# Performance work log

Measured on AMD Instinct MI355X. Metric: run time of the kernel, lower is better.

The kernel has to match this reference:

```python
import jax, jax.numpy as jnp
import numpy as np

N_NODES = 100000
N_EDGES = 3200000
IN_CH = 128
HID_CH = 64
NEG_SLOPE = 0.2  # PyG GATConv default leaky_relu slope


def setup_inputs() -> dict:
    key = jax.random.key(0)
    k1, k2, k3, k4, k5, k6 = jax.random.split(key, 6)
    x = jax.random.normal(k1, (N_NODES, IN_CH), dtype=jnp.float32)
    edge_index = jax.random.randint(k2, (2, N_EDGES), 0, N_NODES, dtype=jnp.int64)
    # learned params of GATConv(in, hid, heads=1)
    W = jax.random.normal(k3, (IN_CH, HID_CH), dtype=jnp.float32) / np.sqrt(IN_CH)
    att_src = jax.random.normal(k4, (HID_CH,), dtype=jnp.float32) / np.sqrt(HID_CH)
    att_dst = jax.random.normal(k5, (HID_CH,), dtype=jnp.float32) / np.sqrt(HID_CH)
    bias = jax.random.normal(k6, (HID_CH,), dtype=jnp.float32) * 0.01
    return {"x": x, "edge_index": edge_index, "W": W, "att_src": att_src,
            "att_dst": att_dst, "bias": bias}


def reference(x, edge_index, W, att_src, att_dst, bias):
    N = x.shape[0]
    h = x @ W  # [N, H] linear transform
    # PyG GATConv default: add self loops
    loops = jnp.arange(N, dtype=edge_index.dtype)
    src = jnp.concatenate([edge_index[0], loops])  # [E+N]
    dst = jnp.concatenate([edge_index[1], loops])
    # per-node attention halves, then gather per-edge
    a_src = h @ att_src  # [N]
    a_dst = h @ att_dst  # [N]
    e = jax.nn.leaky_relu(a_src[src] + a_dst[dst], NEG_SLOPE)  # [E+N]
    # segment softmax over incoming edges of each destination node
    m = jax.ops.segment_max(e, dst, num_segments=N)
    e = jnp.exp(e - m[dst])
    s = jax.ops.segment_sum(e, dst, num_segments=N)
    alpha = e / s[dst]  # [E+N]
    # scatter-aggregate weighted source features
    out = jax.ops.segment_sum(h[src] * alpha[:, None], dst, num_segments=N) + bias
    return out, alpha[:, None]
```

## Files before the change

### kernel.cpp

```cpp
#include <hip/hip_runtime.h>
#include <hip/hip_bf16.h>

#define IN_CH 128
#define HID 64
#define NEG_SLOPE 0.2f
#define BSH 9
#define CAP 18432

typedef __attribute__((ext_vector_type(8))) short short8;
typedef __attribute__((ext_vector_type(4))) float floatx4;

__device__ inline short bfr(float f) {
    unsigned u = __float_as_uint(f);
    u += 0x7fffu + ((u >> 16) & 1u);
    return (short)(u >> 16);
}

__global__ void k_prep(const float* __restrict__ W, short* __restrict__ wfrag)
{
    int idx = blockIdx.x * 256 + threadIdx.x;
    if (idx >= 1024) return;
    int f = idx >> 6, l = idx & 63;
    int kt = f >> 2, nt = f & 3;
    int k0 = kt * 32 + (l >> 4) * 8;
    int n = nt * 16 + (l & 15);
#pragma unroll
    for (int j = 0; j < 8; ++j)
        wfrag[idx * 8 + j] = bfr(W[(k0 + j) * HID + n]);
}

__global__ __launch_bounds__(256) void k_gemm(
    const float* __restrict__ x, const short8* __restrict__ wfrag,
    const float* __restrict__ att_src, const float* __restrict__ att_dst,
    short* __restrict__ h, float* __restrict__ a_src,
    float* __restrict__ a_dst, int N)
{
    const int t = threadIdx.x;
    const int lane = t & 63;
    const int wv = t >> 6;
    const int l15 = lane & 15;
    const int quad = lane >> 4;

    short8 bf[16];
#pragma unroll
    for (int f = 0; f < 16; ++f) bf[f] = wfrag[f * 64 + lane];

    float as4[4], ad4[4];
#pragma unroll
    for (int nt = 0; nt < 4; ++nt) {
        as4[nt] = att_src[nt * 16 + l15];
        ad4[nt] = att_dst[nt * 16 + l15];
    }

    const int rowbase = blockIdx.x * 128 + wv * 32;

#pragma unroll
    for (int mt = 0; mt < 2; ++mt) {
        const int m0 = rowbase + mt * 16;
        const int rowa = m0 + l15;
        const int rowc = rowa < N ? rowa : N - 1;
        const float* xp = x + (size_t)rowc * IN_CH + quad * 8;

        short8 af[4];
#pragma unroll
        for (int kt = 0; kt < 4; ++kt) {
            float4 p0 = *(const float4*)(xp + kt * 32);
            float4 p1 = *(const float4*)(xp + kt * 32 + 4);
            short8 a;
            a[0] = bfr(p0.x); a[1] = bfr(p0.y); a[2] = bfr(p0.z); a[3] = bfr(p0.w);
            a[4] = bfr(p1.x); a[5] = bfr(p1.y); a[6] = bfr(p1.z); a[7] = bfr(p1.w);
            af[kt] = a;
        }

        floatx4 acc[4];
#pragma unroll
        for (int nt = 0; nt < 4; ++nt) acc[nt] = (floatx4){0.f, 0.f, 0.f, 0.f};
#pragma unroll
        for (int kt = 0; kt < 4; ++kt)
#pragma unroll
            for (int nt = 0; nt < 4; ++nt)
                acc[nt] = __builtin_amdgcn_mfma_f32_16x16x32_bf16(
                    af[kt], bf[kt * 4 + nt], acc[nt], 0, 0, 0);

#pragma unroll
        for (int r = 0; r < 4; ++r) {
            const int row = m0 + quad * 4 + r;
            const bool ok = row < N;
            if (ok) {
#pragma unroll
                for (int nt = 0; nt < 4; ++nt)
                    h[(size_t)row * HID + nt * 16 + l15] = bfr(acc[nt][r]);
            }
            float ps = acc[0][r] * as4[0] + acc[1][r] * as4[1] +
                       acc[2][r] * as4[2] + acc[3][r] * as4[3];
            float pd = acc[0][r] * ad4[0] + acc[1][r] * ad4[1] +
                       acc[2][r] * ad4[2] + acc[3][r] * ad4[3];
#pragma unroll
            for (int m2 = 1; m2 < 16; m2 <<= 1) {
                ps += __shfl_xor(ps, m2, 64);
                pd += __shfl_xor(pd, m2, 64);
            }
            if (ok && l15 == 0) { a_src[row] = ps; a_dst[row] = pd; }
        }
    }
}

__global__ __launch_bounds__(256) void k_binB(
    const int* __restrict__ ei, int* __restrict__ g_cursor,
    int* __restrict__ pairs, int E, int nb)
{
    __shared__ int hist[256];
    __shared__ int base[256];
    const int t = threadIdx.x;
    hist[t] = 0;
    __syncthreads();

    int s[16], d[16];
    const int4* s4 = (const int4*)ei;
    const int4* d4 = (const int4*)(ei + E);
    const int E4 = E >> 2;
    const int q0 = blockIdx.x * 1024;
#pragma unroll
    for (int i = 0; i < 4; ++i) {
        int q = q0 + i * 256 + t;
        int4 sv = make_int4(0, 0, 0, 0);
        int4 dv = make_int4(-1, -1, -1, -1);
        if (q < E4) { sv = s4[q]; dv = d4[q]; }
        s[4 * i + 0] = sv.x; s[4 * i + 1] = sv.y; s[4 * i + 2] = sv.z; s[4 * i + 3] = sv.w;
        d[4 * i + 0] = dv.x; d[4 * i + 1] = dv.y; d[4 * i + 2] = dv.z; d[4 * i + 3] = dv.w;
    }
#pragma unroll
    for (int i = 0; i < 16; ++i)
        if (d[i] >= 0) atomicAdd(&hist[d[i] >> BSH], 1);
    __syncthreads();

    if (t < nb) base[t] = atomicAdd(&g_cursor[t], hist[t]);
    __syncthreads();
    hist[t] = 0;
    __syncthreads();

#pragma unroll
    for (int i = 0; i < 16; ++i) {
        if (d[i] < 0) continue;
        int b = d[i] >> BSH;
        int l = atomicAdd(&hist[b], 1);
        int pos = base[b] + l;
        if (pos < CAP)
            pairs[b * CAP + pos] = s[i] | ((d[i] & 511) << 17);
    }
}

__global__ __launch_bounds__(256) void k_bscan(
    const int* __restrict__ g_cursor, int* __restrict__ bucket_base, int nb)
{
    __shared__ int sh[256];
    const int t = threadIdx.x;
    int v = (t < nb) ? g_cursor[t] : 0;
    sh[t] = v;
    __syncthreads();
    for (int off = 1; off < 256; off <<= 1) {
        int u = (t >= off) ? sh[t - off] : 0;
        __syncthreads();
        sh[t] += u;
        __syncthreads();
    }
    if (t < nb) bucket_base[t] = sh[t] - v;
}

__global__ __launch_bounds__(512) void k_binC(
    const int* __restrict__ pairs, const int* __restrict__ g_cursor,
    const int* __restrict__ bucket_base,
    int* __restrict__ row_start, int* __restrict__ cnt,
    int* __restrict__ csr_src, int N)
{
    __shared__ int h0[512];
    __shared__ int hs[512];
    __shared__ int cur[512];
    const int t = threadIdx.x;
    const int b = blockIdx.x;
    const int d0 = b << BSH;
    const int m = g_cursor[b];
    const int basec = bucket_base[b];
    const int* pb = pairs + b * CAP;

    h0[t] = 0;
    __syncthreads();
    for (int i = t; i < m; i += 512)
        atomicAdd(&h0[pb[i] >> 17], 1);
    __syncthreads();

    hs[t] = h0[t];
    __syncthreads();
    for (int off = 1; off < 512; off <<= 1) {
        int u = (t >= off) ? hs[t - off] : 0;
        __syncthreads();
        hs[t] += u;
        __syncthreads();
    }
    const int excl = hs[t] - h0[t];
    cur[t] = basec + excl;
    const int dd = d0 + t;
    if (dd < N) { row_start[dd] = basec + excl; cnt[dd] = h0[t]; }
    __syncthreads();

    for (int i = t; i < m; i += 512) {
        int p = pb[i];
        int pos = atomicAdd(&cur[p >> 17], 1);
        csr_src[pos] = p & 0x1FFFF;
    }
}

__global__ __launch_bounds__(256) void k_agg(
    const __hip_bfloat16* __restrict__ h, const float* __restrict__ a_src,
    const float* __restrict__ a_dst, const float* __restrict__ bias,
    const int* __restrict__ row_start, const int* __restrict__ cnt,
    const int* __restrict__ csr_src,
    float* __restrict__ out, float* __restrict__ inv_s, int N)
{
    const int wave = threadIdx.x >> 6;
    const int lane = threadIdx.x & 63;
    const int d = blockIdx.x * 4 + wave;
    if (d >= N) return;

    const int q  = lane >> 3;
    const int i8 = lane & 7;

    const float ad = a_dst[d];
    const int start = row_start[d];
    const int n = cnt[d];
    const int end = start + n;

    const uint4* h4 = (const uint4*)h;

    float psum = 0.f;
    float acc[8];
#pragma unroll
    for (int c = 0; c < 8; ++c) acc[c] = 0.f;

    for (int b = start; b < end; b += 64) {
        int idx = b + lane;
        int s = 0;
        float e = 0.f;
        if (idx < end) {
            s = csr_src[idx];
            float v = a_src[s] + ad;
            v = v > 0.f ? v : NEG_SLOPE * v;
            e = __expf(v);
            psum += e;
        }
        const int m = min(64, end - b);
#pragma unroll 4
        for (int j = 0; j < m; j += 8) {
            const int jq = j + q;
            const int sj = __shfl(s, jq, 64);
            const float ej = __shfl(e, jq, 64);
            uint4 u = h4[(size_t)sj * 8 + i8];
            acc[0] = fmaf(ej, __uint_as_float(u.x << 16),          acc[0]);
            acc[1] = fmaf(ej, __uint_as_float(u.x & 0xffff0000u),  acc[1]);
            acc[2] = fmaf(ej, __uint_as_float(u.y << 16),          acc[2]);
            acc[3] = fmaf(ej, __uint_as_float(u.y & 0xffff0000u),  acc[3]);
            acc[4] = fmaf(ej, __uint_as_float(u.z << 16),          acc[4]);
            acc[5] = fmaf(ej, __uint_as_float(u.z & 0xffff0000u),  acc[5]);
            acc[6] = fmaf(ej, __uint_as_float(u.w << 16),          acc[6]);
            acc[7] = fmaf(ej, __uint_as_float(u.w & 0xffff0000u),  acc[7]);
        }
    }

#pragma unroll
    for (int m2 = 32; m2 > 0; m2 >>= 1) psum += __shfl_xor(psum, m2, 64);

    float vs = a_src[d] + ad;
    vs = vs > 0.f ? vs : NEG_SLOPE * vs;
    const float eself = __expf(vs);
    const float inv = 1.0f / (psum + eself);
    if (lane == 0) inv_s[d] = inv;

#pragma unroll
    for (int c = 0; c < 8; ++c) {
        acc[c] += __shfl_xor(acc[c], 8, 64);
        acc[c] += __shfl_xor(acc[c], 16, 64);
        acc[c] += __shfl_xor(acc[c], 32, 64);
    }

    if (q == 0) {
        uint4 u = h4[(size_t)d * 8 + i8];
        float hc[8];
        hc[0] = __uint_as_float(u.x << 16);
        hc[1] = __uint_as_float(u.x & 0xffff0000u);
        hc[2] = __uint_as_float(u.y << 16);
        hc[3] = __uint_as_float(u.y & 0xffff0000u);
        hc[4] = __uint_as_float(u.z << 16);
        hc[5] = __uint_as_float(u.z & 0xffff0000u);
        hc[6] = __uint_as_float(u.w << 16);
        hc[7] = __uint_as_float(u.w & 0xffff0000u);
        float4 b0 = ((const float4*)bias)[2 * i8];
        float4 b1 = ((const float4*)bias)[2 * i8 + 1];
        float4 o0, o1;
        o0.x = fmaf(eself, hc[0], acc[0]) * inv + b0.x;
        o0.y = fmaf(eself, hc[1], acc[1]) * inv + b0.y;
        o0.z = fmaf(eself, hc[2], acc[2]) * inv + b0.z;
        o0.w = fmaf(eself, hc[3], acc[3]) * inv + b0.w;
        o1.x = fmaf(eself, hc[4], acc[4]) * inv + b1.x;
        o1.y = fmaf(eself, hc[5], acc[5]) * inv + b1.y;
        o1.z = fmaf(eself, hc[6], acc[6]) * inv + b1.z;
        o1.w = fmaf(eself, hc[7], acc[7]) * inv + b1.w;
        float* op = out + (size_t)d * HID + 8 * i8;
        *(float4*)op       = o0;
        *(float4*)(op + 4) = o1;
    }
}

__global__ void k_alpha(const int* __restrict__ ei,
                        const float* __restrict__ a_src,
                        const float* __restrict__ a_dst,
                        const float* __restrict__ inv_s,
                        float* __restrict__ out_alpha, int E, int N)
{
    int e = blockIdx.x * 256 + threadIdx.x;
    if (e >= E + N) return;
    int s, d;
    if (e < E) { s = ei[e]; d = ei[E + e]; }
    else       { s = e - E; d = s; }
    float v = a_src[s] + a_dst[d];
    v = v > 0.f ? v : NEG_SLOPE * v;
    out_alpha[e] = __expf(v) * inv_s[d];
}

extern "C" void kernel_launch(void* const* d_in, const int* in_sizes, int n_in,
                              void* d_out, int out_size, void* d_ws, size_t ws_size,
                              hipStream_t stream)
{
    (void)n_in; (void)out_size; (void)ws_size;
    const float* x       = (const float*)d_in[0];
    const int*   ei      = (const int*)d_in[1];
    const float* W       = (const float*)d_in[2];
    const float* att_src = (const float*)d_in[3];
    const float* att_dst = (const float*)d_in[4];
    const float* bias    = (const float*)d_in[5];

    const int N = in_sizes[0] / IN_CH;
    const int E = in_sizes[1] / 2;
    const int T = E + N;
    const int nb = (N + 511) >> BSH;

    __hip_bfloat16* h = (__hip_bfloat16*)d_ws;
    float* a_src_d = (float*)(h + (size_t)N * HID);
    float* a_dst_d = a_src_d + N;
    float* inv_s   = a_dst_d + N;
    int* row_start = (int*)(inv_s + N);
    int* cnt       = row_start + N;
    int* g_cursor  = cnt + N;
    int* bucket_b  = g_cursor + 256;
    short* wfrag   = (short*)(bucket_b + 256);
    int* pairs     = (int*)(wfrag + 8192);
    int* csr_src   = pairs + (size_t)nb * CAP;

    float* out       = (float*)d_out;
    float* out_alpha = out + (size_t)N * HID;

    k_prep<<<4, 256, 0, stream>>>(W, wfrag);
    k_gemm<<<(N + 127) / 128, 256, 0, stream>>>(x, (const short8*)wfrag,
                                                att_src, att_dst,
                                                (short*)h, a_src_d, a_dst_d, N);
    hipMemsetAsync(g_cursor, 0, 256 * sizeof(int), stream);
    k_binB<<<(E / 4 + 1023) / 1024, 256, 0, stream>>>(ei, g_cursor, pairs, E, nb);
    k_bscan<<<1, 256, 0, stream>>>(g_cursor, bucket_b, nb);
    k_binC<<<nb, 512, 0, stream>>>(pairs, g_cursor, bucket_b,
                                   row_start, cnt, csr_src, N);
    k_agg<<<(N + 3) / 4, 256, 0, stream>>>(h, a_src_d, a_dst_d, bias,
                                           row_start, cnt, csr_src,
                                           out, inv_s, N);
    k_alpha<<<(T + 255) / 256, 256, 0, stream>>>(ei, a_src_d, a_dst_d, inv_s,
                                                 out_alpha, E, N);
}
```

Measured before the change: 299.5 us.

## Fuse bucket scan into binning, drop memset, process two nodes per wave in aggregation

Removes the separate memset and bucket-scan launches: k_prep zeroes the cursor and every k_binC block recomputes the prefix over bucket counts itself. The aggregation kernel now handles two destination nodes per wave, interleaving their gathers for more memory-level parallelism, and reduces partial sums through LDS instead of shuffles. It also packs a_dst and inv_s into one float2 array so k_alpha does a single gather per edge. The cost is a redundant scan in every binC block, extra registers in agg, and load imbalance when paired nodes have very different degrees.

```diff
diff --git a/kernel.cpp b/kernel.cpp
--- a/kernel.cpp
+++ b/kernel.cpp
@@ -16,8 +16,10 @@
     return (short)(u >> 16);
 }
 
-__global__ void k_prep(const float* __restrict__ W, short* __restrict__ wfrag)
-{
+__global__ void k_prep(const float* __restrict__ W, short* __restrict__ wfrag,
+                       int* __restrict__ g_cursor)
+{
+    if (blockIdx.x == 0) g_cursor[threadIdx.x] = 0;
     int idx = blockIdx.x * 256 + threadIdx.x;
     if (idx >= 1024) return;
     int f = idx >> 6, l = idx & 63;
@@ -150,46 +152,23 @@
     }
 }
 
-__global__ __launch_bounds__(256) void k_bscan(
-    const int* __restrict__ g_cursor, int* __restrict__ bucket_base, int nb)
-{
-    __shared__ int sh[256];
-    const int t = threadIdx.x;
-    int v = (t < nb) ? g_cursor[t] : 0;
-    sh[t] = v;
-    __syncthreads();
-    for (int off = 1; off < 256; off <<= 1) {
-        int u = (t >= off) ? sh[t - off] : 0;
-        __syncthreads();
-        sh[t] += u;
-        __syncthreads();
-    }
-    if (t < nb) bucket_base[t] = sh[t] - v;
-}
-
 __global__ __launch_bounds__(512) void k_binC(
     const int* __restrict__ pairs, const int* __restrict__ g_cursor,
-    const int* __restrict__ bucket_base,
     int* __restrict__ row_start, int* __restrict__ cnt,
-    int* __restrict__ csr_src, int N)
+    int* __restrict__ csr_src, int N, int nb)
 {
     __shared__ int h0[512];
     __shared__ int hs[512];
     __shared__ int cur[512];
+    __shared__ int sbase;
     const int t = threadIdx.x;
     const int b = blockIdx.x;
     const int d0 = b << BSH;
     const int m = g_cursor[b];
-    const int basec = bucket_base[b];
     const int* pb = pairs + b * CAP;
 
-    h0[t] = 0;
-    __syncthreads();
-    for (int i = t; i < m; i += 512)
-        atomicAdd(&h0[pb[i] >> 17], 1);
-    __syncthreads();
-
-    hs[t] = h0[t];
+    int bv = (t < nb) ? g_cursor[t] : 0;
+    hs[t] = bv;
     __syncthreads();
     for (int off = 1; off < 512; off <<= 1) {
         int u = (t >= off) ? hs[t - off] : 0;
@@ -197,6 +176,23 @@
         hs[t] += u;
         __syncthreads();
     }
+    if (t == b) sbase = hs[t] - bv;
+    h0[t] = 0;
+    __syncthreads();
+    const int basec = sbase;
+
+    for (int i = t; i < m; i += 512)
+        atomicAdd(&h0[pb[i] >> 17], 1);
+    __syncthreads();
+
+    hs[t] = h0[t];
+    __syncthreads();
+    for (int off = 1; off < 512; off <<= 1) {
+        int u = (t >= off) ? hs[t - off] : 0;
+        __syncthreads();
+        hs[t] += u;
+        __syncthreads();
+    }
     const int excl = hs[t] - h0[t];
     cur[t] = basec + excl;
     const int dd = d0 + t;
@@ -215,105 +211,140 @@
     const float* __restrict__ a_dst, const float* __restrict__ bias,
     const int* __restrict__ row_start, const int* __restrict__ cnt,
     const int* __restrict__ csr_src,
-    float* __restrict__ out, float* __restrict__ inv_s, int N)
-{
+    float* __restrict__ out, float2* __restrict__ adi, int N)
+{
+    __shared__ float red[4][2][576];
     const int wave = threadIdx.x >> 6;
     const int lane = threadIdx.x & 63;
-    const int d = blockIdx.x * 4 + wave;
-    if (d >= N) return;
+    const int d0 = blockIdx.x * 8 + wave * 2;
+    if (d0 >= N) return;
+    const int d1 = d0 + 1;
+    const bool has1 = d1 < N;
 
     const int q  = lane >> 3;
     const int i8 = lane & 7;
 
-    const float ad = a_dst[d];
-    const int start = row_start[d];
-    const int n = cnt[d];
-    const int end = start + n;
+    const float ad0 = a_dst[d0];
+    const float ad1 = has1 ? a_dst[d1] : 0.f;
+    const int st0 = row_start[d0];
+    const int n0  = cnt[d0];
+    const int en0 = st0 + n0;
+    const int st1 = has1 ? row_start[d1] : 0;
+    const int n1  = has1 ? cnt[d1] : 0;
+    const int en1 = st1 + n1;
 
     const uint4* h4 = (const uint4*)h;
 
-    float psum = 0.f;
-    float acc[8];
-#pragma unroll
-    for (int c = 0; c < 8; ++c) acc[c] = 0.f;
-
-    for (int b = start; b < end; b += 64) {
-        int idx = b + lane;
-        int s = 0;
-        float e = 0.f;
-        if (idx < end) {
-            s = csr_src[idx];
-            float v = a_src[s] + ad;
+    float ps0 = 0.f, ps1 = 0.f;
+    float ac0[8], ac1[8];
+#pragma unroll
+    for (int c = 0; c < 8; ++c) { ac0[c] = 0.f; ac1[c] = 0.f; }
+
+    const int nbt0 = (n0 + 63) >> 6;
+    const int nbt1 = (n1 + 63) >> 6;
+    const int nbm = nbt0 > nbt1 ? nbt0 : nbt1;
+
+    int b0 = st0, b1 = st1;
+    for (int it = 0; it < nbm; ++it, b0 += 64, b1 += 64) {
+        int s0v = 0, s1v = 0;
+        float e0 = 0.f, e1 = 0.f;
+        const int idx0 = b0 + lane;
+        if (it < nbt0 && idx0 < en0) {
+            s0v = csr_src[idx0];
+            float v = a_src[s0v] + ad0;
             v = v > 0.f ? v : NEG_SLOPE * v;
-            e = __expf(v);
-            psum += e;
+            e0 = __expf(v);
+            ps0 += e0;
         }
-        const int m = min(64, end - b);
+        const int idx1 = b1 + lane;
+        if (it < nbt1 && idx1 < en1) {
+            s1v = csr_src[idx1];
+            float v = a_src[s1v] + ad1;
+            v = v > 0.f ? v : NEG_SLOPE * v;
+            e1 = __expf(v);
+            ps1 += e1;
+        }
+        const int m0 = (it < nbt0) ? min(64, en0 - b0) : 0;
+        const int m1 = (it < nbt1) ? min(64, en1 - b1) : 0;
+        const int mm = m0 > m1 ? m0 : m1;
 #pragma unroll 4
-        for (int j = 0; j < m; j += 8) {
+        for (int j = 0; j < mm; j += 8) {
             const int jq = j + q;
-            const int sj = __shfl(s, jq, 64);
-            const float ej = __shfl(e, jq, 64);
-            uint4 u = h4[(size_t)sj * 8 + i8];
-            acc[0] = fmaf(ej, __uint_as_float(u.x << 16),          acc[0]);
-            acc[1] = fmaf(ej, __uint_as_float(u.x & 0xffff0000u),  acc[1]);
-            acc[2] = fmaf(ej, __uint_as_float(u.y << 16),          acc[2]);
-            acc[3] = fmaf(ej, __uint_as_float(u.y & 0xffff0000u),  acc[3]);
-            acc[4] = fmaf(ej, __uint_as_float(u.z << 16),          acc[4]);
-            acc[5] = fmaf(ej, __uint_as_float(u.z & 0xffff0000u),  acc[5]);
-            acc[6] = fmaf(ej, __uint_as_float(u.w << 16),          acc[6]);
-            acc[7] = fmaf(ej, __uint_as_float(u.w & 0xffff0000u),  acc[7]);
+            const int sj0 = __shfl(s0v, jq, 64);
+            const float ej0 = __shfl(e0, jq, 64);
+            const int sj1 = __shfl(s1v, jq, 64);
+            const float ej1 = __shfl(e1, jq, 64);
+            uint4 u0 = h4[(size_t)sj0 * 8 + i8];
+            uint4 u1 = h4[(size_t)sj1 * 8 + i8];
+            ac0[0] = fmaf(ej0, __uint_as_float(u0.x << 16),         ac0[0]);
+            ac0[1] = fmaf(ej0, __uint_as_float(u0.x & 0xffff0000u), ac0[1]);
+            ac0[2] = fmaf(ej0, __uint_as_float(u0.y << 16),         ac0[2]);
+            ac0[3] = fmaf(ej0, __uint_as_float(u0.y & 0xffff0000u), ac0[3]);
+            ac0[4] = fmaf(ej0, __uint_as_float(u0.z << 16),         ac0[4]);
+            ac0[5] = fmaf(ej0, __uint_as_float(u0.z & 0xffff0000u), ac0[5]);
+            ac0[6] = fmaf(ej0, __uint_as_float(u0.w << 16),         ac0[6]);
+            ac0[7] = fmaf(ej0, __uint_as_float(u0.w & 0xffff0000u), ac0[7]);
+            ac1[0] = fmaf(ej1, __uint_as_float(u1.x << 16),         ac1[0]);
+            ac1[1] = fmaf(ej1, __uint_as_float(u1.x & 0xffff0000u), ac1[1]);
+            ac1[2] = fmaf(ej1, __uint_as_float(u1.y << 16),         ac1[2]);
+            ac1[3] = fmaf(ej1, __uint_as_float(u1.y & 0xffff0000u), ac1[3]);
+            ac1[4] = fmaf(ej1, __uint_as_float(u1.z << 16),         ac1[4]);
+            ac1[5] = fmaf(ej1, __uint_as_float(u1.z & 0xffff0000u), ac1[5]);
+            ac1[6] = fmaf(ej1, __uint_as_float(u1.w << 16),         ac1[6]);
+            ac1[7] = fmaf(ej1, __uint_as_float(u1.w & 0xffff0000u), ac1[7]);
         }
     }
 
-#pragma unroll
-    for (int m2 = 32; m2 > 0; m2 >>= 1) psum += __shfl_xor(psum, m2, 64);
-
-    float vs = a_src[d] + ad;
-    vs = vs > 0.f ? vs : NEG_SLOPE * vs;
-    const float eself = __expf(vs);
-    const float inv = 1.0f / (psum + eself);
-    if (lane == 0) inv_s[d] = inv;
-
-#pragma unroll
-    for (int c = 0; c < 8; ++c) {
-        acc[c] += __shfl_xor(acc[c], 8, 64);
-        acc[c] += __shfl_xor(acc[c], 16, 64);
-        acc[c] += __shfl_xor(acc[c], 32, 64);
-    }
-
-    if (q == 0) {
-        uint4 u = h4[(size_t)d * 8 + i8];
-        float hc[8];
-        hc[0] = __uint_as_float(u.x << 16);
-        hc[1] = __uint_as_float(u.x & 0xffff0000u);
-        hc[2] = __uint_as_float(u.y << 16);
-        hc[3] = __uint_as_float(u.y & 0xffff0000u);
-        hc[4] = __uint_as_float(u.z << 16);
-        hc[5] = __uint_as_float(u.z & 0xffff0000u);
-        hc[6] = __uint_as_float(u.w << 16);
-        hc[7] = __uint_as_float(u.w & 0xffff0000u);
-        float4 b0 = ((const float4*)bias)[2 * i8];
-        float4 b1 = ((const float4*)bias)[2 * i8 + 1];
-        float4 o0, o1;
-        o0.x = fmaf(eself, hc[0], acc[0]) * inv + b0.x;
-        o0.y = fmaf(eself, hc[1], acc[1]) * inv + b0.y;
-        o0.z = fmaf(eself, hc[2], acc[2]) * inv + b0.z;
-        o0.w = fmaf(eself, hc[3], acc[3]) * inv + b0.w;
-        o1.x = fmaf(eself, hc[4], acc[4]) * inv + b1.x;
-        o1.y = fmaf(eself, hc[5], acc[5]) * inv + b1.y;
-        o1.z = fmaf(eself, hc[6], acc[6]) * inv + b1.z;
-        o1.w = fmaf(eself, hc[7], acc[7]) * inv + b1.w;
-        float* op = out + (size_t)d * HID + 8 * i8;
-        *(float4*)op       = o0;
-        *(float4*)(op + 4) = o1;
+    float* r0 = &red[wave][0][0];
+    float* r1 = &red[wave][1][0];
+#pragma unroll
+    for (int c = 0; c < 8; ++c) r0[lane * 9 + c] = ac0[c];
+#pragma unroll
+    for (int c = 0; c < 8; ++c) r1[lane * 9 + c] = ac1[c];
+
+#pragma unroll
+    for (int m2 = 32; m2 > 0; m2 >>= 1) {
+        ps0 += __shfl_xor(ps0, m2, 64);
+        ps1 += __shfl_xor(ps1, m2, 64);
+    }
+
+    float vs0 = a_src[d0] + ad0;
+    vs0 = vs0 > 0.f ? vs0 : NEG_SLOPE * vs0;
+    const float es0 = __expf(vs0);
+    const float inv0 = 1.f / (ps0 + es0);
+    float es1 = 0.f, inv1 = 0.f;
+    if (has1) {
+        float vs1 = a_src[d1] + ad1;
+        vs1 = vs1 > 0.f ? vs1 : NEG_SLOPE * vs1;
+        es1 = __expf(vs1);
+        inv1 = 1.f / (ps1 + es1);
+    }
+    if (lane == 0) {
+        adi[d0] = make_float2(ad0, inv0);
+        if (has1) adi[d1] = make_float2(ad1, inv1);
+    }
+
+    const int oi = lane >> 3, oc = lane & 7;
+    float s0 = 0.f, s1 = 0.f;
+#pragma unroll
+    for (int qq = 0; qq < 8; ++qq) {
+        s0 += r0[(qq * 8 + oi) * 9 + oc];
+        s1 += r1[(qq * 8 + oi) * 9 + oc];
+    }
+
+    const ushort* hu = (const ushort*)h;
+    const float bi = bias[lane];
+    float hs0 = __uint_as_float(((unsigned)hu[(size_t)d0 * HID + lane]) << 16);
+    out[(size_t)d0 * HID + lane] = fmaf(es0, hs0, s0) * inv0 + bi;
+    if (has1) {
+        float hs1 = __uint_as_float(((unsigned)hu[(size_t)d1 * HID + lane]) << 16);
+        out[(size_t)d1 * HID + lane] = fmaf(es1, hs1, s1) * inv1 + bi;
     }
 }
 
 __global__ void k_alpha(const int* __restrict__ ei,
                         const float* __restrict__ a_src,
-                        const float* __restrict__ a_dst,
-                        const float* __restrict__ inv_s,
+                        const float2* __restrict__ adi,
                         float* __restrict__ out_alpha, int E, int N)
 {
     int e = blockIdx.x * 256 + threadIdx.x;
@@ -321,9 +352,10 @@
     int s, d;
     if (e < E) { s = ei[e]; d = ei[E + e]; }
     else       { s = e - E; d = s; }
-    float v = a_src[s] + a_dst[d];
+    float2 av = adi[d];
+    float v = a_src[s] + av.x;
     v = v > 0.f ? v : NEG_SLOPE * v;
-    out_alpha[e] = __expf(v) * inv_s[d];
+    out_alpha[e] = __expf(v) * av.y;
 }
 
 extern "C" void kernel_launch(void* const* d_in, const int* in_sizes, int n_in,
@@ -346,30 +378,27 @@
     __hip_bfloat16* h = (__hip_bfloat16*)d_ws;
     float* a_src_d = (float*)(h + (size_t)N * HID);
     float* a_dst_d = a_src_d + N;
-    float* inv_s   = a_dst_d + N;
-    int* row_start = (int*)(inv_s + N);
+    float2* adi    = (float2*)(a_dst_d + N);
+    int* row_start = (int*)(adi + N);
     int* cnt       = row_start + N;
     int* g_cursor  = cnt + N;
-    int* bucket_b  = g_cursor + 256;
-    short* wfrag   = (short*)(bucket_b + 256);
+    short* wfrag   = (short*)(g_cursor + 256);
     int* pairs     = (int*)(wfrag + 8192);
     int* csr_src   = pairs + (size_t)nb * CAP;
 
     float* out       = (float*)d_out;
     float* out_alpha = out + (size_t)N * HID;
 
-    k_prep<<<4, 256, 0, stream>>>(W, wfrag);
+    k_prep<<<4, 256, 0, stream>>>(W, wfrag, g_cursor);
     k_gemm<<<(N + 127) / 128, 256, 0, stream>>>(x, (const short8*)wfrag,
                                                 att_src, att_dst,
                                                 (short*)h, a_src_d, a_dst_d, N);
-    hipMemsetAsync(g_cursor, 0, 256 * sizeof(int), stream);
     k_binB<<<(E / 4 + 1023) / 1024, 256, 0, stream>>>(ei, g_cursor, pairs, E, nb);
-    k_bscan<<<1, 256, 0, stream>>>(g_cursor, bucket_b, nb);
-    k_binC<<<nb, 512, 0, stream>>>(pairs, g_cursor, bucket_b,
-                                   row_start, cnt, csr_src, N);
-    k_agg<<<(N + 3) / 4, 256, 0, stream>>>(h, a_src_d, a_dst_d, bias,
+    k_binC<<<nb, 512, 0, stream>>>(pairs, g_cursor,
+                                   row_start, cnt, csr_src, N, nb);
+    k_agg<<<(N + 7) / 8, 256, 0, stream>>>(h, a_src_d, a_dst_d, bias,
                                            row_start, cnt, csr_src,
-                                           out, inv_s, N);
-    k_alpha<<<(T + 255) / 256, 256, 0, stream>>>(ei, a_src_d, a_dst_d, inv_s,
+                                           out, adi, N);
+    k_alpha<<<(T + 255) / 256, 256, 0, stream>>>(ei, a_src_d, adi,
                                                  out_alpha, E, N);
 }
```

Measured after the change: 273.3 us. 8.7% less time.
